# Kernel tuning notes

Measured on AMD Instinct MI355X. Metric: run time of the kernel, lower is better.

The kernel has to match this reference:

```python
import jax, jax.numpy as jnp
import numpy as np

B, SENSORY, UNITS, MOTOR = 4096, 64, 128, 32
ODE_UNFOLDS = 6
EPSILON = 1e-8
ELAPSED_TIME = 1.0


def setup_inputs() -> dict:
    key = jax.random.key(0)
    ks = jax.random.split(key, 16)
    u = lambda k, shape, lo, hi: jax.random.uniform(k, shape, jnp.float32, lo, hi)
    return {
        "inputs": jax.random.normal(ks[0], (B, SENSORY), jnp.float32),
        "state": jax.random.normal(ks[1], (B, UNITS), jnp.float32),
        "gleak": u(ks[2], (UNITS,), 0.001, 1.0),
        "vleak": u(ks[3], (UNITS,), -0.2, 0.2),
        "cm": u(ks[4], (UNITS,), 0.4, 0.6),
        "sigma": u(ks[5], (UNITS, UNITS), 3.0, 8.0),
        "mu": u(ks[6], (UNITS, UNITS), 0.3, 0.8),
        "w": u(ks[7], (UNITS, UNITS), 0.001, 1.0),
        "erev": jnp.sign(jax.random.normal(ks[8], (UNITS, UNITS), jnp.float32)),
        "sensory_sigma": u(ks[9], (SENSORY, UNITS), 3.0, 8.0),
        "sensory_mu": u(ks[10], (SENSORY, UNITS), 0.3, 0.8),
        "sensory_w": u(ks[11], (SENSORY, UNITS), 0.001, 1.0),
        "sensory_erev": jnp.sign(jax.random.normal(ks[12], (SENSORY, UNITS), jnp.float32)),
        "input_w": jnp.ones((SENSORY,), jnp.float32),
        "input_b": jnp.zeros((SENSORY,), jnp.float32),
        "output_w": jnp.ones((MOTOR,), jnp.float32),
        "output_b": jnp.zeros((MOTOR,), jnp.float32),
        "sparsity_mask": jax.random.randint(ks[13], (UNITS, UNITS), 0, 2) > 0,
        "sensory_sparsity_mask": jax.random.randint(ks[14], (SENSORY, UNITS), 0, 2) > 0,
    }


def reference(inputs, state, gleak, vleak, cm, sigma, mu, w, erev,
              sensory_sigma, sensory_mu, sensory_w, sensory_erev,
              input_w, input_b, output_w, output_b,
              sparsity_mask, sensory_sparsity_mask):
    mask = sparsity_mask.astype(jnp.float32)
    smask = sensory_sparsity_mask.astype(jnp.float32)

    # input mapping (affine)
    x = inputs * input_w + input_b  # [B, sensory]

    # sensory synapse activation: [B, sensory, units]
    sens_act = sensory_w * jax.nn.sigmoid(sensory_sigma * (x[:, :, None] - sensory_mu)) * smask
    w_num_sensory = jnp.sum(sens_act * sensory_erev, axis=1)  # [B, units]
    w_den_sensory = jnp.sum(sens_act, axis=1)                 # [B, units]

    cm_t = cm / (ELAPSED_TIME / ODE_UNFOLDS)  # [units]

    def step(v_pre, _):
        # [B, units, units] broadcasted synapse activation
        wa = w * jax.nn.sigmoid(sigma * (v_pre[:, :, None] - mu)) * mask
        w_num = jnp.sum(wa * erev, axis=1) + w_num_sensory
        w_den = jnp.sum(wa, axis=1) + w_den_sensory
        numerator = cm_t * v_pre + gleak * vleak + w_num
        denominator = cm_t + gleak + w_den
        return numerator / (denominator + EPSILON), None

    next_state, _ = jax.lax.scan(step, state, None, length=ODE_UNFOLDS)

    # output mapping: slice motor neurons, affine
    out = next_state[:, :MOTOR] * output_w + output_b
    return out, next_state
```

## Files before the change

kernel.cpp:

```cpp
#include <hip/hip_runtime.h>

#define BATCH    4096
#define SENS     64
#define UNITS    128
#define MOTOR_N  32
#define UNFOLDS  6
#define NB       4
#define ROWS_PER_BLOCK 16
#define NBLOCKS  (BATCH / ROWS_PER_BLOCK)
#define NGROUPS  (ROWS_PER_BLOCK / NB)
#define VP 140
#define XP 68

#define LOG2E 1.4426950408889634f

__device__ __forceinline__ float fast_exp2(float x) { return __builtin_amdgcn_exp2f(x); }
__device__ __forceinline__ float fast_rcp(float x)  { return __builtin_amdgcn_rcpf(x); }
__device__ __forceinline__ unsigned f2bf(float x) {
    unsigned v = __float_as_uint(x);
    v += 0x7fffu + ((v >> 16) & 1u);
    return v >> 16;
}
__device__ __forceinline__ float bf_lo(unsigned p) { return __uint_as_float(p << 16); }
__device__ __forceinline__ float bf_hi(unsigned p) { return __uint_as_float(p & 0xffff0000u); }
__device__ __forceinline__ int vpad(int j) { return j + ((j >> 5) << 2); }

__global__ __launch_bounds__(1024)
void ltc_fused(
    const float* __restrict__ inputs,  const float* __restrict__ state,
    const float* __restrict__ gleak,   const float* __restrict__ vleak,
    const float* __restrict__ cm,
    const float* __restrict__ sigma,   const float* __restrict__ mu,
    const float* __restrict__ w,       const float* __restrict__ erev,
    const float* __restrict__ s_sigma, const float* __restrict__ s_mu,
    const float* __restrict__ s_w,     const float* __restrict__ s_erev,
    const float* __restrict__ input_w, const float* __restrict__ input_b,
    const float* __restrict__ output_w,const float* __restrict__ output_b,
    const int*   __restrict__ mask,    const int* __restrict__ s_mask,
    float* __restrict__ out, float* __restrict__ next_state)
{
    __shared__ __align__(16) float x_lds[ROWS_PER_BLOCK][XP];
    __shared__ float nb_lds[ROWS_PER_BLOCK][UNITS];
    __shared__ float db_lds[ROWS_PER_BLOCK][UNITS];
    __shared__ __align__(16) float v_lds[2][NB][VP];

    const int t = threadIdx.x;
    const int u = t >> 3;
    const int c = t & 7;
    const int vread = c * 16 + ((c >> 1) << 2);
    const int xread = c * 8  + ((c >> 2) << 2);

    const float cmt = cm[u] * 6.0f;
    const float glv = gleak[u];
    const float nb0 = glv * vleak[u];
    const float db0 = cmt + glv + 1e-8f;

    {
        const int r = t >> 6, s = t & 63;
        x_lds[r][vpad(s) == s + ((s >> 5) << 2) ? s + ((s >> 5) << 2) : 0] =
            0.0f;
        x_lds[r][s + ((s >> 5) << 2)] =
            inputs[(blockIdx.x * ROWS_PER_BLOCK + r) * SENS + s] * input_w[s] + input_b[s];
    }

    float sgl[8], sgb[8];
    unsigned swsp[4];
#pragma unroll
    for (int k2 = 0; k2 < 4; ++k2) {
        float wt[2];
#pragma unroll
        for (int e = 0; e < 2; ++e) {
            int k = k2 * 2 + e;
            int idx = (c * 8 + k) * UNITS + u;
            float sg = s_sigma[idx] * LOG2E;
            float wv = s_w[idx] * (s_mask[idx] != 0 ? 1.0f : 0.0f);
            sgl[k] = -sg;
            sgb[k] = sg * s_mu[idx];
            wt[e]  = wv * s_erev[idx];
        }
        swsp[k2] = (f2bf(wt[1]) << 16) | f2bf(wt[0]);
    }
    __syncthreads();

#pragma unroll 1
    for (int row = 0; row < ROWS_PER_BLOCK; ++row) {
        const float4* xp = (const float4*)&x_lds[row][xread];
        float4 xa = xp[0], xb = xp[1];
        float xs[8] = {xa.x, xa.y, xa.z, xa.w, xb.x, xb.y, xb.z, xb.w};
        float nsum = 0.f, dsum = 0.f;
#pragma unroll
        for (int k = 0; k < 8; ++k) {
            float e  = fast_exp2(fmaf(sgl[k], xs[k], sgb[k]));
            float r  = fast_rcp(1.0f + e);
            float ws = (k & 1) ? bf_hi(swsp[k >> 1]) : bf_lo(swsp[k >> 1]);
            nsum = fmaf(ws, r, nsum);
            dsum = fmaf(fabsf(ws), r, dsum);
        }
        nsum += __shfl_xor(nsum, 1, 8);
        nsum += __shfl_xor(nsum, 2, 8);
        nsum += __shfl_xor(nsum, 4, 8);
        dsum += __shfl_xor(dsum, 1, 8);
        dsum += __shfl_xor(dsum, 2, 8);
        dsum += __shfl_xor(dsum, 4, 8);
        if (c == 0) {
            nb_lds[row][u] = nb0 + nsum;
            db_lds[row][u] = db0 + dsum;
        }
    }

    float rgl[16], rgb[16];
    unsigned rwsp[8];
#pragma unroll
    for (int k2 = 0; k2 < 8; ++k2) {
        float wt[2];
#pragma unroll
        for (int e = 0; e < 2; ++e) {
            int k = k2 * 2 + e;
            int idx = (c * 16 + k) * UNITS + u;
            float sg = sigma[idx] * LOG2E;
            float wv = w[idx] * (mask[idx] != 0 ? 1.0f : 0.0f);
            rgl[k] = -sg;
            rgb[k] = sg * mu[idx];
            wt[e]  = wv * erev[idx];
        }
        rwsp[k2] = (f2bf(wt[1]) << 16) | f2bf(wt[0]);
    }
#pragma unroll
    for (int k = 0; k < 16; ++k)
        asm volatile("" : "+v"(rgl[k]), "+v"(rgb[k]));
#pragma unroll
    for (int k2 = 0; k2 < 8; ++k2)
        asm volatile("" : "+v"(rwsp[k2]));

    __syncthreads();

#pragma unroll 1
    for (int g = 0; g < NGROUPS; ++g) {
        const int b0 = blockIdx.x * ROWS_PER_BLOCK + g * NB;
        if (t < NB * UNITS) {
            int b = t >> 7, j = t & 127;
            v_lds[0][b][vpad(j)] = state[(b0 + b) * UNITS + j];
        }
        __syncthreads();

        float vc[NB];
#pragma unroll
        for (int b = 0; b < NB; ++b) vc[b] = v_lds[0][b][vpad(u)];

        int p = 0;
#pragma unroll 1
        for (int step = 0; step < UNFOLDS; ++step) {
#pragma unroll
            for (int b = 0; b < NB; ++b) {
                const float4* vp4 = (const float4*)&v_lds[p][b][vread];
                float nsum = 0.f, dsum = 0.f;
#pragma unroll
                for (int q = 0; q < 4; ++q) {
                    float4 v4 = vp4[q];
                    const float* vf = (const float*)&v4;
#pragma unroll
                    for (int jj = 0; jj < 4; ++jj) {
                        int k = q * 4 + jj;
                        float e  = fast_exp2(fmaf(rgl[k], vf[jj], rgb[k]));
                        float r  = fast_rcp(1.0f + e);
                        float ws = (k & 1) ? bf_hi(rwsp[k >> 1]) : bf_lo(rwsp[k >> 1]);
                        nsum = fmaf(ws, r, nsum);
                        dsum = fmaf(fabsf(ws), r, dsum);
                    }
                }
                nsum += __shfl_xor(nsum, 1, 8);
                nsum += __shfl_xor(nsum, 2, 8);
                nsum += __shfl_xor(nsum, 4, 8);
                dsum += __shfl_xor(dsum, 1, 8);
                dsum += __shfl_xor(dsum, 2, 8);
                dsum += __shfl_xor(dsum, 4, 8);
                const int row = g * NB + b;
                float vnew = fmaf(cmt, vc[b], nsum + nb_lds[row][u])
                           * fast_rcp(dsum + db_lds[row][u]);
                vc[b] = vnew;
                if (c == 0) v_lds[p ^ 1][b][vpad(u)] = vnew;
            }
            __syncthreads();
            p ^= 1;
        }

        if (c == 0) {
#pragma unroll
            for (int b = 0; b < NB; ++b) {
                const int row = b0 + b;
                next_state[row * UNITS + u] = vc[b];
                if (u < MOTOR_N)
                    out[row * MOTOR_N + u] = vc[b] * output_w[u] + output_b[u];
            }
        }
    }
}

extern "C" void kernel_launch(void* const* d_in, const int* in_sizes, int n_in,
                              void* d_out, int out_size, void* d_ws, size_t ws_size,
                              hipStream_t stream) {
    const float* inputs   = (const float*)d_in[0];
    const float* state    = (const float*)d_in[1];
    const float* gleak    = (const float*)d_in[2];
    const float* vleak    = (const float*)d_in[3];
    const float* cm       = (const float*)d_in[4];
    const float* sigma    = (const float*)d_in[5];
    const float* mu       = (const float*)d_in[6];
    const float* w        = (const float*)d_in[7];
    const float* erev     = (const float*)d_in[8];
    const float* s_sigma  = (const float*)d_in[9];
    const float* s_mu     = (const float*)d_in[10];
    const float* s_w      = (const float*)d_in[11];
    const float* s_erev   = (const float*)d_in[12];
    const float* input_w  = (const float*)d_in[13];
    const float* input_b  = (const float*)d_in[14];
    const float* output_w = (const float*)d_in[15];
    const float* output_b = (const float*)d_in[16];
    const int*   mask     = (const int*)d_in[17];
    const int*   s_mask   = (const int*)d_in[18];

    float* out        = (float*)d_out;
    float* next_state = out + (size_t)BATCH * MOTOR_N;

    ltc_fused<<<NBLOCKS, 1024, 0, stream>>>(
        inputs, state, gleak, vleak, cm, sigma, mu, w, erev,
        s_sigma, s_mu, s_w, s_erev, input_w, input_b, output_w, output_b,
        mask, s_mask, out, next_state);
}
```

Baseline: 222.5 us.

## Use DPP lane reductions, halve rows per block, and repad LDS layouts

Replaces the three-step __shfl_xor reductions across each 8-lane group with DPP-based adds (quad_perm swaps plus row_half_mirror), so partial sums are combined without LDS-backed permutes. Halves ROWS_PER_BLOCK to 8, doubling the grid to 512 blocks, which spreads work across more CUs at the cost of reloading the weights in twice as many blocks. It also repads the v and x LDS arrays to new strides to change bank access patterns, keeps the sensory weights in fp32 instead of packed bf16, and drops one redundant __syncthreads.

```diff
diff --git a/kernel.cpp b/kernel.cpp
--- a/kernel.cpp
+++ b/kernel.cpp
@@ -6,11 +6,9 @@
 #define MOTOR_N  32
 #define UNFOLDS  6
 #define NB       4
-#define ROWS_PER_BLOCK 16
+#define ROWS_PER_BLOCK 8
 #define NBLOCKS  (BATCH / ROWS_PER_BLOCK)
 #define NGROUPS  (ROWS_PER_BLOCK / NB)
-#define VP 140
-#define XP 68
 
 #define LOG2E 1.4426950408889634f
 
@@ -23,7 +21,23 @@
 }
 __device__ __forceinline__ float bf_lo(unsigned p) { return __uint_as_float(p << 16); }
 __device__ __forceinline__ float bf_hi(unsigned p) { return __uint_as_float(p & 0xffff0000u); }
-__device__ __forceinline__ int vpad(int j) { return j + ((j >> 5) << 2); }
+
+__device__ __forceinline__ int vpad(int j) { return j + ((j >> 4) << 2); }
+#define VROW 156
+__device__ __forceinline__ int xpad(int j) { return j + ((j >> 3) << 2); }
+#define XROW 92
+
+template <int CTRL>
+__device__ __forceinline__ float dpp_add(float x) {
+    int s = __builtin_amdgcn_update_dpp(0, __float_as_int(x), CTRL, 0xf, 0xf, true);
+    return x + __int_as_float(s);
+}
+__device__ __forceinline__ float reduce8(float x) {
+    x = dpp_add<0xB1>(x);
+    x = dpp_add<0x4E>(x);
+    x = dpp_add<0x141>(x);
+    return x;
+}
 
 __global__ __launch_bounds__(1024)
 void ltc_fused(
@@ -39,72 +53,58 @@
     const int*   __restrict__ mask,    const int* __restrict__ s_mask,
     float* __restrict__ out, float* __restrict__ next_state)
 {
-    __shared__ __align__(16) float x_lds[ROWS_PER_BLOCK][XP];
+    __shared__ __align__(16) float x_lds[ROWS_PER_BLOCK][XROW];
     __shared__ float nb_lds[ROWS_PER_BLOCK][UNITS];
     __shared__ float db_lds[ROWS_PER_BLOCK][UNITS];
-    __shared__ __align__(16) float v_lds[2][NB][VP];
+    __shared__ __align__(16) float v_lds[2][NB][VROW];
 
     const int t = threadIdx.x;
     const int u = t >> 3;
     const int c = t & 7;
-    const int vread = c * 16 + ((c >> 1) << 2);
-    const int xread = c * 8  + ((c >> 2) << 2);
+    const int vbase = c * 20;
+    const int xbase = c * 12;
 
     const float cmt = cm[u] * 6.0f;
     const float glv = gleak[u];
     const float nb0 = glv * vleak[u];
     const float db0 = cmt + glv + 1e-8f;
 
-    {
-        const int r = t >> 6, s = t & 63;
-        x_lds[r][vpad(s) == s + ((s >> 5) << 2) ? s + ((s >> 5) << 2) : 0] =
-            0.0f;
-        x_lds[r][s + ((s >> 5) << 2)] =
+    if (t < ROWS_PER_BLOCK * SENS) {
+        int r = t >> 6, s = t & 63;
+        x_lds[r][xpad(s)] =
             inputs[(blockIdx.x * ROWS_PER_BLOCK + r) * SENS + s] * input_w[s] + input_b[s];
     }
 
-    float sgl[8], sgb[8];
-    unsigned swsp[4];
-#pragma unroll
-    for (int k2 = 0; k2 < 4; ++k2) {
-        float wt[2];
-#pragma unroll
-        for (int e = 0; e < 2; ++e) {
-            int k = k2 * 2 + e;
-            int idx = (c * 8 + k) * UNITS + u;
-            float sg = s_sigma[idx] * LOG2E;
-            float wv = s_w[idx] * (s_mask[idx] != 0 ? 1.0f : 0.0f);
-            sgl[k] = -sg;
-            sgb[k] = sg * s_mu[idx];
-            wt[e]  = wv * s_erev[idx];
-        }
-        swsp[k2] = (f2bf(wt[1]) << 16) | f2bf(wt[0]);
+    float sgl[8], sgb[8], sws[8];
+#pragma unroll
+    for (int k = 0; k < 8; ++k) {
+        int idx = (c * 8 + k) * UNITS + u;
+        float sg = s_sigma[idx] * LOG2E;
+        float wv = s_w[idx] * (s_mask[idx] != 0 ? 1.0f : 0.0f);
+        sgl[k] = -sg;
+        sgb[k] = sg * s_mu[idx];
+        sws[k] = wv * s_erev[idx];
     }
     __syncthreads();
 
 #pragma unroll 1
     for (int row = 0; row < ROWS_PER_BLOCK; ++row) {
-        const float4* xp = (const float4*)&x_lds[row][xread];
-        float4 xa = xp[0], xb = xp[1];
-        float xs[8] = {xa.x, xa.y, xa.z, xa.w, xb.x, xb.y, xb.z, xb.w};
-        float nsum = 0.f, dsum = 0.f;
+        const float4* xp = (const float4*)&x_lds[row][xbase];
+        float4 xa = xp[0], xb2 = xp[1];
+        float xs[8] = {xa.x, xa.y, xa.z, xa.w, xb2.x, xb2.y, xb2.z, xb2.w};
+        float n = 0.f, d = 0.f;
 #pragma unroll
         for (int k = 0; k < 8; ++k) {
-            float e  = fast_exp2(fmaf(sgl[k], xs[k], sgb[k]));
-            float r  = fast_rcp(1.0f + e);
-            float ws = (k & 1) ? bf_hi(swsp[k >> 1]) : bf_lo(swsp[k >> 1]);
-            nsum = fmaf(ws, r, nsum);
-            dsum = fmaf(fabsf(ws), r, dsum);
-        }
-        nsum += __shfl_xor(nsum, 1, 8);
-        nsum += __shfl_xor(nsum, 2, 8);
-        nsum += __shfl_xor(nsum, 4, 8);
-        dsum += __shfl_xor(dsum, 1, 8);
-        dsum += __shfl_xor(dsum, 2, 8);
-        dsum += __shfl_xor(dsum, 4, 8);
+            float e = fast_exp2(fmaf(sgl[k], xs[k], sgb[k]));
+            float r = fast_rcp(1.0f + e);
+            n = fmaf(sws[k], r, n);
+            d = fmaf(fabsf(sws[k]), r, d);
+        }
+        n = reduce8(n);
+        d = reduce8(d);
         if (c == 0) {
-            nb_lds[row][u] = nb0 + nsum;
-            db_lds[row][u] = db0 + dsum;
+            nb_lds[row][u] = nb0 + n;
+            db_lds[row][u] = db0 + d;
         }
     }
 
@@ -114,25 +114,21 @@
     for (int k2 = 0; k2 < 8; ++k2) {
         float wt[2];
 #pragma unroll
-        for (int e = 0; e < 2; ++e) {
-            int k = k2 * 2 + e;
+        for (int e2 = 0; e2 < 2; ++e2) {
+            int k = k2 * 2 + e2;
             int idx = (c * 16 + k) * UNITS + u;
             float sg = sigma[idx] * LOG2E;
             float wv = w[idx] * (mask[idx] != 0 ? 1.0f : 0.0f);
             rgl[k] = -sg;
             rgb[k] = sg * mu[idx];
-            wt[e]  = wv * erev[idx];
+            wt[e2] = wv * erev[idx];
         }
         rwsp[k2] = (f2bf(wt[1]) << 16) | f2bf(wt[0]);
     }
 #pragma unroll
-    for (int k = 0; k < 16; ++k)
-        asm volatile("" : "+v"(rgl[k]), "+v"(rgb[k]));
-#pragma unroll
-    for (int k2 = 0; k2 < 8; ++k2)
-        asm volatile("" : "+v"(rwsp[k2]));
-
-    __syncthreads();
+    for (int k = 0; k < 16; ++k) asm volatile("" : "+v"(rgl[k]), "+v"(rgb[k]));
+#pragma unroll
+    for (int k2 = 0; k2 < 8; ++k2) asm volatile("" : "+v"(rwsp[k2]));
 
 #pragma unroll 1
     for (int g = 0; g < NGROUPS; ++g) {
@@ -152,31 +148,27 @@
         for (int step = 0; step < UNFOLDS; ++step) {
 #pragma unroll
             for (int b = 0; b < NB; ++b) {
-                const float4* vp4 = (const float4*)&v_lds[p][b][vread];
-                float nsum = 0.f, dsum = 0.f;
-#pragma unroll
-                for (int q = 0; q < 4; ++q) {
-                    float4 v4 = vp4[q];
-                    const float* vf = (const float*)&v4;
-#pragma unroll
-                    for (int jj = 0; jj < 4; ++jj) {
-                        int k = q * 4 + jj;
+                const float4* vp4 = (const float4*)&v_lds[p][b][vbase];
+                float n = 0.f, d = 0.f;
+#pragma unroll
+                for (int h = 0; h < 2; ++h) {
+                    float4 va = vp4[h * 2], vb = vp4[h * 2 + 1];
+                    float vf[8] = {va.x, va.y, va.z, va.w, vb.x, vb.y, vb.z, vb.w};
+#pragma unroll
+                    for (int jj = 0; jj < 8; ++jj) {
+                        int k = h * 8 + jj;
                         float e  = fast_exp2(fmaf(rgl[k], vf[jj], rgb[k]));
                         float r  = fast_rcp(1.0f + e);
                         float ws = (k & 1) ? bf_hi(rwsp[k >> 1]) : bf_lo(rwsp[k >> 1]);
-                        nsum = fmaf(ws, r, nsum);
-                        dsum = fmaf(fabsf(ws), r, dsum);
+                        n = fmaf(ws, r, n);
+                        d = fmaf(fabsf(ws), r, d);
                     }
                 }
-                nsum += __shfl_xor(nsum, 1, 8);
-                nsum += __shfl_xor(nsum, 2, 8);
-                nsum += __shfl_xor(nsum, 4, 8);
-                dsum += __shfl_xor(dsum, 1, 8);
-                dsum += __shfl_xor(dsum, 2, 8);
-                dsum += __shfl_xor(dsum, 4, 8);
+                n = reduce8(n);
+                d = reduce8(d);
                 const int row = g * NB + b;
-                float vnew = fmaf(cmt, vc[b], nsum + nb_lds[row][u])
-                           * fast_rcp(dsum + db_lds[row][u]);
+                float vnew = fmaf(cmt, vc[b], n + nb_lds[row][u])
+                           * fast_rcp(d + db_lds[row][u]);
                 vc[b] = vnew;
                 if (c == 0) v_lds[p ^ 1][b][vpad(u)] = vnew;
             }
```

After: 244.4 us. 1.1x slower.
